# Performance work log

Hardware: AMD Instinct MI355X
Metric: run time of the kernel (lower is better)

Reference implementation:

```python
import jax, jax.numpy as jnp
import numpy as np
import math

B, R, D = 1, 2, 256
NH, NL, NP, ZA = 8, 1, 8, 4
H = W = 128
Q = H * W
HD = D // NH


def _bilinear(v, loc, Hl, Wl):
    # v: [BH, Hl*Wl, hd]; loc: [BH, Q, P, 2] normalized to [0,1]
    x = loc[..., 0] * Wl - 0.5
    y = loc[..., 1] * Hl - 0.5
    x0f = jnp.floor(x); y0f = jnp.floor(y)
    wx = (x - x0f)[..., None]; wy = (y - y0f)[..., None]
    x0 = x0f.astype(jnp.int32); y0 = y0f.astype(jnp.int32)
    def corner(iy, ix):
        valid = (iy >= 0) & (iy < Hl) & (ix >= 0) & (ix < Wl)
        idx = jnp.clip(iy, 0, Hl - 1) * Wl + jnp.clip(ix, 0, Wl - 1)
        g = jax.vmap(lambda vb, ib: vb[ib])(v, idx)  # [BH,Q,P,hd]
        return g * valid[..., None].astype(v.dtype)
    g00 = corner(y0, x0); g01 = corner(y0, x0 + 1)
    g10 = corner(y0 + 1, x0); g11 = corner(y0 + 1, x0 + 1)
    return (g00 * (1 - wx) + g01 * wx) * (1 - wy) + (g10 * (1 - wx) + g11 * wx) * wy


def setup_inputs() -> dict:
    key = jax.random.key(0)
    ks = jax.random.split(key, 12)
    query = jax.random.normal(ks[0], (B, Q, D), jnp.float32)
    value = jax.random.normal(ks[1], (B * R, Q, D), jnp.float32)
    reference_points = jax.random.uniform(ks[2], (R, Q, ZA, 2), jnp.float32)
    spatial_shapes = jnp.array([[H, W]], jnp.int32)
    # sampling_offsets: zero-ish weight + directional grid bias (as in init_weights)
    W_off = 0.01 * jax.random.normal(ks[3], (NH * NL * NP * 2, D), jnp.float32)
    thetas = jnp.arange(NH, dtype=jnp.float32) * (2.0 * math.pi / NH)
    grid = jnp.stack([jnp.cos(thetas), jnp.sin(thetas)], -1)
    grid = grid / jnp.max(jnp.abs(grid), axis=-1, keepdims=True)
    grid = jnp.tile(grid[:, None, None, :], (1, NL, NP, 1))
    grid = grid * (jnp.arange(1, NP + 1, dtype=jnp.float32)[None, None, :, None])
    b_off = grid.reshape(-1)
    W_attn = 0.01 * jax.random.normal(ks[4], (NH * NL * NP, D), jnp.float32)
    b_attn = 0.01 * jax.random.normal(ks[5], (NH * NL * NP,), jnp.float32)
    s = 1.0 / np.sqrt(D)
    W_val = s * jax.random.normal(ks[6], (D, D), jnp.float32)
    b_val = jnp.zeros((D,), jnp.float32)
    W_out = s * jax.random.normal(ks[7], (D, D), jnp.float32)
    b_out = jnp.zeros((D,), jnp.float32)
    return {"query": query, "value": value, "reference_points": reference_points,
            "spatial_shapes": spatial_shapes, "W_off": W_off, "b_off": b_off,
            "W_attn": W_attn, "b_attn": b_attn, "W_val": W_val, "b_val": b_val,
            "W_out": W_out, "b_out": b_out}


def reference(query, value, reference_points, spatial_shapes,
              W_off, b_off, W_attn, b_attn, W_val, b_val, W_out, b_out):
    shapes = np.asarray(spatial_shapes)  # static level shapes
    residual = query
    Bq, nq, d = query.shape
    Rr, _, za, _ = reference_points.shape
    # rebatch query/reference_points over histories -> batch Bq*Rr (== value batch)
    q = jnp.broadcast_to(query[:, None], (Bq, Rr, nq, d)).reshape(Bq * Rr, nq, d)
    rp = jnp.broadcast_to(reference_points[None], (Bq, Rr, nq, za, 2)).reshape(Bq * Rr, nq, za, 2)
    bs = value.shape[0]
    v = (value @ W_val.T + b_val).reshape(bs, -1, NH, HD)
    off = (q @ W_off.T + b_off).reshape(bs, nq, NH, NL, NP, 2)
    aw = jax.nn.softmax((q @ W_attn.T + b_attn).reshape(bs, nq, NH, NL * NP), axis=-1)
    aw = aw.reshape(bs, nq, NH, NL, NP)
    norm = jnp.stack([shapes[:, 1].astype(np.float32), shapes[:, 0].astype(np.float32)], -1)  # [NL,2] = (W,H)
    off = off / norm[None, None, None, :, None, :]
    off = off.reshape(bs, nq, NH, NL, NP // za, za, 2)
    loc = rp[:, :, None, None, None, :, :] + off  # [bs,nq,NH,NL,NP//za,za,2]
    loc = loc.reshape(bs, nq, NH, NL, NP, 2)
    # multi-scale deformable attention (gather + bilinear + weighted sum)
    starts = np.concatenate([[0], np.cumsum(shapes[:, 0] * shapes[:, 1])])
    out = jnp.zeros((bs * NH, nq, HD), v.dtype)
    for l in range(NL):
        Hl, Wl = int(shapes[l, 0]), int(shapes[l, 1])
        vl = v[:, starts[l]:starts[l + 1]].transpose(0, 2, 1, 3).reshape(bs * NH, Hl * Wl, HD)
        locl = loc[:, :, :, l].transpose(0, 2, 1, 3, 4).reshape(bs * NH, nq, NP, 2)
        sampled = _bilinear(vl, locl, Hl, Wl)  # [bs*NH, nq, NP, hd]
        awl = aw[:, :, :, l].transpose(0, 2, 1, 3).reshape(bs * NH, nq, NP)
        out = out + jnp.einsum('bqph,bqp->bqh', sampled, awl)
    out = out.reshape(bs, NH, nq, HD).transpose(0, 2, 1, 3).reshape(bs, nq, d)
    out = out.mean(0, keepdims=True)  # mean over history-batch dim -> [1,nq,d]
    out = out @ W_out.T + b_out
    return out + residual  # dropout is identity in eval
```

## Files before the change

kernel.cpp:

```cpp
#include <hip/hip_runtime.h>
#include <hip/hip_bf16.h>
#include <hip/hip_fp16.h>

#define QN 16384
#define DK 256

typedef float f4_t __attribute__((ext_vector_type(4)));
typedef short s16x8 __attribute__((ext_vector_type(8)));
typedef short s16x4 __attribute__((ext_vector_type(4)));
typedef unsigned int u32;
typedef u32 u32x4 __attribute__((ext_vector_type(4)));
typedef __fp16 h2_t __attribute__((ext_vector_type(2)));

__device__ inline short f2bf(float f){
  __hip_bfloat16 h = __float2bfloat16(f);
  return __builtin_bit_cast(short, h);
}
__device__ inline short f2h16(float f){
  __half h = __float2half(f);
  return __builtin_bit_cast(short, h);
}
__device__ inline float dot2h(u32 a, u32 b, float c){
#if __has_builtin(__builtin_amdgcn_fdot2)
  return __builtin_amdgcn_fdot2(__builtin_bit_cast(h2_t, a),
                                __builtin_bit_cast(h2_t, b), c, false);
#else
  h2_t ha = __builtin_bit_cast(h2_t, a), hb = __builtin_bit_cast(h2_t, b);
  return c + (float)ha[0] * (float)hb[0] + (float)ha[1] * (float)hb[1];
#endif
}
__device__ inline u32 pk2h(float a, float b){
#if __has_builtin(__builtin_amdgcn_cvt_pkrtz)
  h2_t r = __builtin_amdgcn_cvt_pkrtz(a, b);
  return __builtin_bit_cast(u32, r);
#else
  return (u32)__builtin_bit_cast(unsigned short, __float2half(a)) |
         ((u32)__builtin_bit_cast(unsigned short, __float2half(b)) << 16);
#endif
}
__device__ inline u32 bperm(u32 s0, u32 s1, u32 sel){
  return __builtin_amdgcn_perm(s0, s1, sel);
}

__global__ __launch_bounds__(256) void k_convw(const float* __restrict__ Wv,
    const float* __restrict__ Woff, const float* __restrict__ Wattn,
    const float* __restrict__ Wout, short* __restrict__ Wbf){
  const int row = blockIdx.x;
  const int c = threadIdx.x;
  const float* src;
  if (row < 256)       src = Wv    + (size_t)row * DK;
  else if (row < 384)  src = Woff  + (size_t)(row - 256) * DK;
  else if (row < 448)  src = Wattn + (size_t)(row - 384) * DK;
  else                 src = Wout  + (size_t)(row - 448) * DK;
  Wbf[(size_t)row * DK + c] = f2bf(src[c]);
}

__global__ __launch_bounds__(256, 2) void k_gemm_val(const float* __restrict__ A,
    const short* __restrict__ Bw, const float* __restrict__ bval,
    short* __restrict__ vhf){
  __shared__ short As[64 * 256];
  __shared__ short Bs[64 * 256];
  const int tid = threadIdx.x;
  const int lane = tid & 63, wv = tid >> 6;
  const int r16 = lane & 15, kh = lane >> 4;
  const int swsel = (r16 & 7) << 4;
  const int mbase = blockIdx.x * 64;

  #pragma unroll
  for (int i = 0; i < 16; ++i){
    const int lin = i * 256 + tid;
    const int r = lin >> 6, ck = lin & 63;
    const f4_t v = *(const f4_t*)(A + (size_t)(mbase + r) * DK + ck * 4);
    s16x4 o = { f2bf(v[0]), f2bf(v[1]), f2bf(v[2]), f2bf(v[3]) };
    *(s16x4*)((char*)As + r * 512 + ((ck * 8) ^ ((r & 7) << 4))) = o;
  }
  s16x8 breg[8];
  #pragma unroll
  for (int i = 0; i < 8; ++i){
    const int lin = i * 256 + tid;
    const int n = lin >> 5, ck = lin & 31;
    breg[i] = *(const s16x8*)(Bw + (size_t)n * DK + ck * 8);
  }
  __syncthreads();

  for (int cg = 0; cg < 4; ++cg){
    #pragma unroll
    for (int i = 0; i < 8; ++i){
      const int lin = i * 256 + tid;
      const int n = lin >> 5, ck = lin & 31;
      *(s16x8*)((char*)Bs + n * 512 + ((ck * 16) ^ ((n & 7) << 4))) = breg[i];
    }
    __syncthreads();
    if (cg < 3){
      #pragma unroll
      for (int i = 0; i < 8; ++i){
        const int lin = i * 256 + tid;
        const int n = lin >> 5, ck = lin & 31;
        breg[i] = *(const s16x8*)(Bw + (size_t)((cg + 1) * 64 + n) * DK + ck * 8);
      }
    }
    f4_t acc[4];
    #pragma unroll
    for (int i = 0; i < 4; ++i) acc[i] = (f4_t){0.f, 0.f, 0.f, 0.f};
    #pragma unroll
    for (int kk = 0; kk < 8; ++kk){
      const int kb = kh * 16 + kk * 64;
      const s16x8 a = *(const s16x8*)((char*)As + (wv * 16 + r16) * 512 + (kb ^ swsel));
      #pragma unroll
      for (int nt = 0; nt < 4; ++nt){
        const s16x8 b = *(const s16x8*)((char*)Bs + (nt * 16 + r16) * 512 + (kb ^ swsel));
        acc[nt] = __builtin_amdgcn_mfma_f32_16x16x32_bf16(a, b, acc[nt], 0, 0, 0);
      }
    }
    #pragma unroll
    for (int nt = 0; nt < 4; ++nt){
      const int n = cg * 64 + nt * 16 + r16;
      const int h = n >> 5, hd = n & 31;
      const float bv = bval[n];
      #pragma unroll
      for (int rix = 0; rix < 4; ++rix){
        const int m = mbase + wv * 16 + kh * 4 + rix;
        const int r = m >> 14, pix = m & (QN - 1);
        vhf[(size_t)((r * 8 + h) * QN + pix) * 32 + hd] = f2h16(acc[nt][rix] + bv);
      }
    }
    __syncthreads();
  }
}

__global__ __launch_bounds__(256, 2) void k_gemm_oa(const float* __restrict__ A,
    const short* __restrict__ Bw, const float* __restrict__ boff,
    const float* __restrict__ battn, float* __restrict__ offw,
    float* __restrict__ logit){
  __shared__ short As[32 * 256];
  __shared__ short Bs[64 * 256];
  const int tid = threadIdx.x;
  const int lane = tid & 63, wv = tid >> 6;
  const int r16 = lane & 15, kh = lane >> 4;
  const int mg = wv & 1, ch = wv >> 1;
  const int swsel = (r16 & 7) << 4;
  const int mbase = blockIdx.x * 32;

  #pragma unroll
  for (int i = 0; i < 8; ++i){
    const int lin = i * 256 + tid;
    const int r = lin >> 6, ck = lin & 63;
    const f4_t v = *(const f4_t*)(A + (size_t)(mbase + r) * DK + ck * 4);
    s16x4 o = { f2bf(v[0]), f2bf(v[1]), f2bf(v[2]), f2bf(v[3]) };
    *(s16x4*)((char*)As + r * 512 + ((ck * 8) ^ ((r & 7) << 4))) = o;
  }
  s16x8 breg[8];
  #pragma unroll
  for (int i = 0; i < 8; ++i){
    const int lin = i * 256 + tid;
    const int n = lin >> 5, ck = lin & 31;
    breg[i] = *(const s16x8*)(Bw + (size_t)n * DK + ck * 8);
  }
  __syncthreads();

  for (int cg = 0; cg < 3; ++cg){
    #pragma unroll
    for (int i = 0; i < 8; ++i){
      const int lin = i * 256 + tid;
      const int n = lin >> 5, ck = lin & 31;
      *(s16x8*)((char*)Bs + n * 512 + ((ck * 16) ^ ((n & 7) << 4))) = breg[i];
    }
    __syncthreads();
    if (cg < 2){
      #pragma unroll
      for (int i = 0; i < 8; ++i){
        const int lin = i * 256 + tid;
        const int n = lin >> 5, ck = lin & 31;
        breg[i] = *(const s16x8*)(Bw + (size_t)((cg + 1) * 64 + n) * DK + ck * 8);
      }
    }
    f4_t acc[2];
    acc[0] = (f4_t){0.f,0.f,0.f,0.f}; acc[1] = (f4_t){0.f,0.f,0.f,0.f};
    #pragma unroll
    for (int kk = 0; kk < 8; ++kk){
      const int kb = kh * 16 + kk * 64;
      const s16x8 a = *(const s16x8*)((char*)As + (mg * 16 + r16) * 512 + (kb ^ swsel));
      #pragma unroll
      for (int nt = 0; nt < 2; ++nt){
        const s16x8 b = *(const s16x8*)((char*)Bs + (ch * 32 + nt * 16 + r16) * 512 + (kb ^ swsel));
        acc[nt] = __builtin_amdgcn_mfma_f32_16x16x32_bf16(a, b, acc[nt], 0, 0, 0);
      }
    }
    #pragma unroll
    for (int nt = 0; nt < 2; ++nt){
      const int n = cg * 64 + ch * 32 + nt * 16 + r16;
      #pragma unroll
      for (int rix = 0; rix < 4; ++rix){
        const int m = mbase + mg * 16 + kh * 4 + rix;
        const float v = acc[nt][rix];
        if (n < 128) offw[(size_t)m * 128 + n] = v + boff[n];
        else         logit[(size_t)m * 64 + (n - 128)] = v + battn[n - 128];
      }
    }
    __syncthreads();
  }
}

__global__ __launch_bounds__(256, 2) void k_gemm_out(const float* __restrict__ A,
    const short* __restrict__ Bw, const float* __restrict__ bout,
    const float* __restrict__ query, float* __restrict__ out){
  __shared__ short As[32 * 256];
  __shared__ short Bs[64 * 256];
  const int tid = threadIdx.x;
  const int lane = tid & 63, wv = tid >> 6;
  const int r16 = lane & 15, kh = lane >> 4;
  const int mg = wv & 1, ch = wv >> 1;
  const int swsel = (r16 & 7) << 4;
  const int mbase = blockIdx.x * 32;

  #pragma unroll
  for (int i = 0; i < 8; ++i){
    const int lin = i * 256 + tid;
    const int r = lin >> 6, ck = lin & 63;
    const f4_t v = *(const f4_t*)(A + (size_t)(mbase + r) * DK + ck * 4);
    s16x4 o = { f2bf(v[0]), f2bf(v[1]), f2bf(v[2]), f2bf(v[3]) };
    *(s16x4*)((char*)As + r * 512 + ((ck * 8) ^ ((r & 7) << 4))) = o;
  }
  s16x8 breg[8];
  #pragma unroll
  for (int i = 0; i < 8; ++i){
    const int lin = i * 256 + tid;
    const int n = lin >> 5, ck = lin & 31;
    breg[i] = *(const s16x8*)(Bw + (size_t)n * DK + ck * 8);
  }
  __syncthreads();

  for (int cg = 0; cg < 4; ++cg){
    #pragma unroll
    for (int i = 0; i < 8; ++i){
      const int lin = i * 256 + tid;
      const int n = lin >> 5, ck = lin & 31;
      *(s16x8*)((char*)Bs + n * 512 + ((ck * 16) ^ ((n & 7) << 4))) = breg[i];
    }
    __syncthreads();
    if (cg < 3){
      #pragma unroll
      for (int i = 0; i < 8; ++i){
        const int lin = i * 256 + tid;
        const int n = lin >> 5, ck = lin & 31;
        breg[i] = *(const s16x8*)(Bw + (size_t)((cg + 1) * 64 + n) * DK + ck * 8);
      }
    }
    f4_t acc[2];
    acc[0] = (f4_t){0.f,0.f,0.f,0.f}; acc[1] = (f4_t){0.f,0.f,0.f,0.f};
    #pragma unroll
    for (int kk = 0; kk < 8; ++kk){
      const int kb = kh * 16 + kk * 64;
      const s16x8 a = *(const s16x8*)((char*)As + (mg * 16 + r16) * 512 + (kb ^ swsel));
      #pragma unroll
      for (int nt = 0; nt < 2; ++nt){
        const s16x8 b = *(const s16x8*)((char*)Bs + (ch * 32 + nt * 16 + r16) * 512 + (kb ^ swsel));
        acc[nt] = __builtin_amdgcn_mfma_f32_16x16x32_bf16(a, b, acc[nt], 0, 0, 0);
      }
    }
    #pragma unroll
    for (int nt = 0; nt < 2; ++nt){
      const int n = cg * 64 + ch * 32 + nt * 16 + r16;
      const float bo = bout[n];
      #pragma unroll
      for (int rix = 0; rix < 4; ++rix){
        const int m = mbase + mg * 16 + kh * 4 + rix;
        out[(size_t)m * DK + n] = acc[nt][rix] + bo + query[(size_t)m * DK + n];
      }
    }
    __syncthreads();
  }
}

__device__ inline void mkw(float rx, float ry, float ox, float oy, float awp,
                           u32& word, u32& pk01, u32& pk23){
  const float x = fmaf(rx, 128.f, ox) - 0.5f;
  const float y = fmaf(ry, 128.f, oy) - 0.5f;
  const float xf = floorf(x), yf = floorf(y);
  const float wx = x - xf, wy = y - yf;
  const int ix = (int)xf, iy = (int)yf;
  float xw0 = 1.f - wx, xw1 = wx, yw0 = 1.f - wy, yw1 = wy;
  if (ix < 0 || ix > 127)   xw0 = 0.f;
  if (ix < -1 || ix > 126)  xw1 = 0.f;
  if (iy < 0 || iy > 127)   yw0 = 0.f;
  if (iy < -1 || iy > 126)  yw1 = 0.f;
  const int ix0 = min(max(ix, 0), 127), ix1 = min(max(ix + 1, 0), 127);
  const int iy0 = min(max(iy, 0), 127), iy1 = min(max(iy + 1, 0), 127);
  const float t0 = awp * yw0, t1 = awp * yw1;
  pk01 = pk2h(t0 * xw0, t0 * xw1);
  pk23 = pk2h(t1 * xw0, t1 * xw1);
  word = (u32)(iy0 * 128 + ix0) | ((u32)(ix1 - ix0) << 16) | ((u32)(iy1 - iy0) << 17);
}

__global__ __launch_bounds__(256) void k_sampler(const float* __restrict__ rp,
    const float* __restrict__ offw, const float* __restrict__ logit,
    const short* __restrict__ vhf, float* __restrict__ O2){
  const int tid = threadIdx.x;
  const int j = tid & 3;
  const int grp = tid >> 2;
  const int lane = tid & 63;
  const int glane = lane & ~3;
  const int h = blockIdx.x & 7;
  const int q = (blockIdx.x >> 3) * 64 + grp;
  const u32 jof = (u32)j * 8;

  const float* lp = logit + (size_t)q * 64 + h * 8;
  const float l0 = lp[0], l1 = lp[1], l2 = lp[2], l3 = lp[3];
  const float l4 = lp[4], l5 = lp[5], l6 = lp[6], l7 = lp[7];
  float mx = fmaxf(fmaxf(fmaxf(l0, l1), fmaxf(l2, l3)),
                   fmaxf(fmaxf(l4, l5), fmaxf(l6, l7)));
  float sum = __expf(l0 - mx) + __expf(l1 - mx) + __expf(l2 - mx) + __expf(l3 - mx)
            + __expf(l4 - mx) + __expf(l5 - mx) + __expf(l6 - mx) + __expf(l7 - mx);
  const float sc = 0.5f / sum;
  const float wA = __expf(lp[j] - mx) * sc;
  const float wB = __expf(lp[j + 4] - mx) * sc;

  const float* offp = offw + (size_t)q * 128 + h * 16;
  const float ox0 = offp[2 * j],     oy0 = offp[2 * j + 1];
  const float ox1 = offp[2 * j + 8], oy1 = offp[2 * j + 9];
  const float* rp0 = rp + (size_t)q * 8 + j * 2;
  const float* rp1 = rp + (size_t)(QN + q) * 8 + j * 2;
  const float rx0 = rp0[0], ry0 = rp0[1];
  const float rx1 = rp1[0], ry1 = rp1[1];

  u32 wrd0, pk01_0, pk23_0, wrd1, pk01_1, pk23_1;
  u32 wrd2, pk01_2, pk23_2, wrd3, pk01_3, pk23_3;
  mkw(rx0, ry0, ox0, oy0, wA, wrd0, pk01_0, pk23_0);
  mkw(rx0, ry0, ox1, oy1, wB, wrd1, pk01_1, pk23_1);
  mkw(rx1, ry1, ox0, oy0, wA, wrd2, pk01_2, pk23_2);
  mkw(rx1, ry1, ox1, oy1, wB, wrd3, pk01_3, pk23_3);

  const short* vb0 = vhf + (size_t)(h * QN) * 32;
  const short* vb1 = vhf + (size_t)((8 + h) * QN) * 32;

  float acc[8] = {0.f,0.f,0.f,0.f,0.f,0.f,0.f,0.f};

#define STEP(S, WRD, PK01, PK23) do{                                        \
    const int srcl_ = glane | ((S) & 3);                                    \
    const u32 w01_ = __shfl((PK01), srcl_);                                 \
    const u32 w23_ = __shfl((PK23), srcl_);                                 \
    const u32 wd_  = __shfl((WRD),  srcl_);                                 \
    const u32 o00_ = (wd_ & 0xFFFFu) * 32u + jof;                           \
    const u32 o01_ = o00_ + ((wd_ >> 11) & 32u);                            \
    const u32 dy_  = (wd_ >> 17) & 1u;                                      \
    const u32 o10_ = o00_ + dy_ * 4096u;                                    \
    const u32 o11_ = o01_ + dy_ * 4096u;                                    \
    const short* vb_ = ((S) >> 3) ? vb1 : vb0;                              \
    const u32x4 c00_ = *(const u32x4*)(vb_ + o00_);                         \
    const u32x4 c01_ = *(const u32x4*)(vb_ + o01_);                         \
    const u32x4 c10_ = *(const u32x4*)(vb_ + o10_);                         \
    const u32x4 c11_ = *(const u32x4*)(vb_ + o11_);                         \
    _Pragma("unroll")                                                       \
    for (int e = 0; e < 4; ++e){                                            \
      const u32 p0_ = bperm(c01_[e], c00_[e], 0x05040100u);                 \
      const u32 p1_ = bperm(c01_[e], c00_[e], 0x07060302u);                 \
      const u32 q0_ = bperm(c11_[e], c10_[e], 0x05040100u);                 \
      const u32 q1_ = bperm(c11_[e], c10_[e], 0x07060302u);                 \
      acc[2*e]   = dot2h(p0_, w01_, acc[2*e]);                              \
      acc[2*e+1] = dot2h(p1_, w01_, acc[2*e+1]);                            \
      acc[2*e]   = dot2h(q0_, w23_, acc[2*e]);                              \
      acc[2*e+1] = dot2h(q1_, w23_, acc[2*e+1]);                            \
    }                                                                       \
  }while(0)

  STEP(0,  wrd0, pk01_0, pk23_0); STEP(1,  wrd0, pk01_0, pk23_0);
  STEP(2,  wrd0, pk01_0, pk23_0); STEP(3,  wrd0, pk01_0, pk23_0);
  STEP(4,  wrd1, pk01_1, pk23_1); STEP(5,  wrd1, pk01_1, pk23_1);
  STEP(6,  wrd1, pk01_1, pk23_1); STEP(7,  wrd1, pk01_1, pk23_1);
  STEP(8,  wrd2, pk01_2, pk23_2); STEP(9,  wrd2, pk01_2, pk23_2);
  STEP(10, wrd2, pk01_2, pk23_2); STEP(11, wrd2, pk01_2, pk23_2);
  STEP(12, wrd3, pk01_3, pk23_3); STEP(13, wrd3, pk01_3, pk23_3);
  STEP(14, wrd3, pk01_3, pk23_3); STEP(15, wrd3, pk01_3, pk23_3);
#undef STEP

  float* op = O2 + (size_t)q * DK + h * 32 + j * 8;
  *(f4_t*)op       = (f4_t){acc[0], acc[1], acc[2], acc[3]};
  *(f4_t*)(op + 4) = (f4_t){acc[4], acc[5], acc[6], acc[7]};
}

extern "C" void kernel_launch(void* const* d_in, const int* in_sizes, int n_in,
                              void* d_out, int out_size, void* d_ws, size_t ws_size,
                              hipStream_t stream) {
  const float* query = (const float*)d_in[0];
  const float* value = (const float*)d_in[1];
  const float* refpt = (const float*)d_in[2];
  const float* W_off  = (const float*)d_in[4];
  const float* b_off  = (const float*)d_in[5];
  const float* W_attn = (const float*)d_in[6];
  const float* b_attn = (const float*)d_in[7];
  const float* W_val  = (const float*)d_in[8];
  const float* b_val  = (const float*)d_in[9];
  const float* W_out  = (const float*)d_in[10];
  const float* b_out  = (const float*)d_in[11];
  float* out = (float*)d_out;

  char* ws = (char*)d_ws;
  short* Wbf  = (short*)(ws);
  short* vhf  = (short*)(ws + 360448);
  float* offw = (float*)(ws + 17137664);
  float* logit= (float*)(ws + 25526272);
  float* O2   = (float*)(ws + 29720576);

  k_convw   <<<dim3(704),  dim3(256), 0, stream>>>(W_val, W_off, W_attn, W_out, Wbf);
  k_gemm_val<<<dim3(512),  dim3(256), 0, stream>>>(value, Wbf, b_val, vhf);
  k_gemm_oa <<<dim3(512),  dim3(256), 0, stream>>>(query, Wbf + 256 * DK, b_off, b_attn, offw, logit);
  k_sampler <<<dim3(2048), dim3(256), 0, stream>>>(refpt, offw, logit, vhf, O2);
  k_gemm_out<<<dim3(512),  dim3(256), 0, stream>>>(O2, Wbf + 448 * DK, b_out, query, out);
}
```

Measured before the change: 79.37 us.

## Split sampler corner gathers across lane pairs and store bf16 intermediate

The sampler now assigns 8 threads per query-head instead of 4. Each lane pair splits the x-corners of a sample, so every lane loads two corners instead of four, and the partial sums are combined with a shuffle. The softmax over the 8 logits becomes a shuffle reduction, and the grid doubles to 4096 blocks. The sampler output is also written as bf16 instead of fp32, which halves that write and lets the output GEMM load bf16 directly without converting. In exchange the kernel does more shuffles and half the lanes sit idle at the store.

```diff
diff --git a/kernel.cpp b/kernel.cpp
--- a/kernel.cpp
+++ b/kernel.cpp
@@ -201,7 +201,7 @@
   }
 }
 
-__global__ __launch_bounds__(256, 2) void k_gemm_out(const float* __restrict__ A,
+__global__ __launch_bounds__(256, 2) void k_gemm_out(const short* __restrict__ Ab,
     const short* __restrict__ Bw, const float* __restrict__ bout,
     const float* __restrict__ query, float* __restrict__ out){
   __shared__ short As[32 * 256];
@@ -214,12 +214,11 @@
   const int mbase = blockIdx.x * 32;
 
   #pragma unroll
-  for (int i = 0; i < 8; ++i){
-    const int lin = i * 256 + tid;
-    const int r = lin >> 6, ck = lin & 63;
-    const f4_t v = *(const f4_t*)(A + (size_t)(mbase + r) * DK + ck * 4);
-    s16x4 o = { f2bf(v[0]), f2bf(v[1]), f2bf(v[2]), f2bf(v[3]) };
-    *(s16x4*)((char*)As + r * 512 + ((ck * 8) ^ ((r & 7) << 4))) = o;
+  for (int i = 0; i < 4; ++i){
+    const int lin = i * 256 + tid;
+    const int r = lin >> 5, ck = lin & 31;
+    const s16x8 v = *(const s16x8*)(Ab + (size_t)(mbase + r) * DK + ck * 8);
+    *(s16x8*)((char*)As + r * 512 + ((ck * 16) ^ ((r & 7) << 4))) = v;
   }
   s16x8 breg[8];
   #pragma unroll
@@ -294,88 +293,80 @@
 
 __global__ __launch_bounds__(256) void k_sampler(const float* __restrict__ rp,
     const float* __restrict__ offw, const float* __restrict__ logit,
-    const short* __restrict__ vhf, float* __restrict__ O2){
+    const short* __restrict__ vhf, short* __restrict__ O2b){
   const int tid = threadIdx.x;
-  const int j = tid & 3;
-  const int grp = tid >> 2;
+  const int j3 = tid & 7;
+  const int cj = j3 & 3;
+  const int px = j3 >> 2;
+  const int grp = tid >> 3;
   const int lane = tid & 63;
-  const int glane = lane & ~3;
+  const int glane8 = lane & ~7;
   const int h = blockIdx.x & 7;
-  const int q = (blockIdx.x >> 3) * 64 + grp;
-  const u32 jof = (u32)j * 8;
+  const int q = (blockIdx.x >> 3) * 32 + grp;
+  const u32 cjof = (u32)cj * 8;
+  const u32 selw = px ? 0x03020706u : 0x01000504u;
 
   const float* lp = logit + (size_t)q * 64 + h * 8;
-  const float l0 = lp[0], l1 = lp[1], l2 = lp[2], l3 = lp[3];
-  const float l4 = lp[4], l5 = lp[5], l6 = lp[6], l7 = lp[7];
-  float mx = fmaxf(fmaxf(fmaxf(l0, l1), fmaxf(l2, l3)),
-                   fmaxf(fmaxf(l4, l5), fmaxf(l6, l7)));
-  float sum = __expf(l0 - mx) + __expf(l1 - mx) + __expf(l2 - mx) + __expf(l3 - mx)
-            + __expf(l4 - mx) + __expf(l5 - mx) + __expf(l6 - mx) + __expf(l7 - mx);
-  const float sc = 0.5f / sum;
-  const float wA = __expf(lp[j] - mx) * sc;
-  const float wB = __expf(lp[j + 4] - mx) * sc;
+  const float l = lp[j3];
+  float m = l;
+  m = fmaxf(m, __shfl_xor(m, 1)); m = fmaxf(m, __shfl_xor(m, 2)); m = fmaxf(m, __shfl_xor(m, 4));
+  const float e = __expf(l - m);
+  float ssum = e;
+  ssum += __shfl_xor(ssum, 1); ssum += __shfl_xor(ssum, 2); ssum += __shfl_xor(ssum, 4);
+  const float awp = e * (0.5f / ssum);
 
   const float* offp = offw + (size_t)q * 128 + h * 16;
-  const float ox0 = offp[2 * j],     oy0 = offp[2 * j + 1];
-  const float ox1 = offp[2 * j + 8], oy1 = offp[2 * j + 9];
-  const float* rp0 = rp + (size_t)q * 8 + j * 2;
-  const float* rp1 = rp + (size_t)(QN + q) * 8 + j * 2;
-  const float rx0 = rp0[0], ry0 = rp0[1];
-  const float rx1 = rp1[0], ry1 = rp1[1];
-
-  u32 wrd0, pk01_0, pk23_0, wrd1, pk01_1, pk23_1;
-  u32 wrd2, pk01_2, pk23_2, wrd3, pk01_3, pk23_3;
-  mkw(rx0, ry0, ox0, oy0, wA, wrd0, pk01_0, pk23_0);
-  mkw(rx0, ry0, ox1, oy1, wB, wrd1, pk01_1, pk23_1);
-  mkw(rx1, ry1, ox0, oy0, wA, wrd2, pk01_2, pk23_2);
-  mkw(rx1, ry1, ox1, oy1, wB, wrd3, pk01_3, pk23_3);
+  const float ox = offp[2 * j3], oy = offp[2 * j3 + 1];
+  const int za2 = (j3 & 3) * 2;
+  const float rx0 = rp[(size_t)q * 8 + za2],        ry0 = rp[(size_t)q * 8 + za2 + 1];
+  const float rx1 = rp[(size_t)(QN + q) * 8 + za2], ry1 = rp[(size_t)(QN + q) * 8 + za2 + 1];
+
+  u32 wrdA, pkA01, pkA23, wrdB, pkB01, pkB23;
+  mkw(rx0, ry0, ox, oy, awp, wrdA, pkA01, pkA23);
+  mkw(rx1, ry1, ox, oy, awp, wrdB, pkB01, pkB23);
 
   const short* vb0 = vhf + (size_t)(h * QN) * 32;
   const short* vb1 = vhf + (size_t)((8 + h) * QN) * 32;
 
   float acc[8] = {0.f,0.f,0.f,0.f,0.f,0.f,0.f,0.f};
 
-#define STEP(S, WRD, PK01, PK23) do{                                        \
-    const int srcl_ = glane | ((S) & 3);                                    \
+#define STEP(S, WRD, PK01, PK23, VB) do{                                    \
+    const int srcl_ = glane8 | ((S) & 7);                                   \
+    const u32 wd_  = __shfl((WRD),  srcl_);                                 \
     const u32 w01_ = __shfl((PK01), srcl_);                                 \
     const u32 w23_ = __shfl((PK23), srcl_);                                 \
-    const u32 wd_  = __shfl((WRD),  srcl_);                                 \
-    const u32 o00_ = (wd_ & 0xFFFFu) * 32u + jof;                           \
-    const u32 o01_ = o00_ + ((wd_ >> 11) & 32u);                            \
-    const u32 dy_  = (wd_ >> 17) & 1u;                                      \
-    const u32 o10_ = o00_ + dy_ * 4096u;                                    \
-    const u32 o11_ = o01_ + dy_ * 4096u;                                    \
-    const short* vb_ = ((S) >> 3) ? vb1 : vb0;                              \
-    const u32x4 c00_ = *(const u32x4*)(vb_ + o00_);                         \
-    const u32x4 c01_ = *(const u32x4*)(vb_ + o01_);                         \
-    const u32x4 c10_ = *(const u32x4*)(vb_ + o10_);                         \
-    const u32x4 c11_ = *(const u32x4*)(vb_ + o11_);                         \
+    const u32 wp_  = bperm(w01_, w23_, selw);     \
+    const u32 o0_  = (wd_ & 0xFFFFu) * 32u + cjof                           \
+                   + (px ? ((wd_ >> 11) & 32u) : 0u);                       \
+    const u32 o1_  = o0_ + ((wd_ >> 17) & 1u) * 4096u;                      \
+    const u32x4 cA_ = *(const u32x4*)((VB) + o0_);              \
+    const u32x4 cB_ = *(const u32x4*)((VB) + o1_);              \
     _Pragma("unroll")                                                       \
-    for (int e = 0; e < 4; ++e){                                            \
-      const u32 p0_ = bperm(c01_[e], c00_[e], 0x05040100u);                 \
-      const u32 p1_ = bperm(c01_[e], c00_[e], 0x07060302u);                 \
-      const u32 q0_ = bperm(c11_[e], c10_[e], 0x05040100u);                 \
-      const u32 q1_ = bperm(c11_[e], c10_[e], 0x07060302u);                 \
-      acc[2*e]   = dot2h(p0_, w01_, acc[2*e]);                              \
-      acc[2*e+1] = dot2h(p1_, w01_, acc[2*e+1]);                            \
-      acc[2*e]   = dot2h(q0_, w23_, acc[2*e]);                              \
-      acc[2*e+1] = dot2h(q1_, w23_, acc[2*e+1]);                            \
+    for (int e_ = 0; e_ < 4; ++e_){                                         \
+      const u32 pl_ = bperm(cA_[e_], cB_[e_], 0x01000504u);                 \
+      const u32 ph_ = bperm(cA_[e_], cB_[e_], 0x03020706u);                 \
+      acc[2*e_]   = dot2h(pl_, wp_, acc[2*e_]);                             \
+      acc[2*e_+1] = dot2h(ph_, wp_, acc[2*e_+1]);                           \
     }                                                                       \
   }while(0)
 
-  STEP(0,  wrd0, pk01_0, pk23_0); STEP(1,  wrd0, pk01_0, pk23_0);
-  STEP(2,  wrd0, pk01_0, pk23_0); STEP(3,  wrd0, pk01_0, pk23_0);
-  STEP(4,  wrd1, pk01_1, pk23_1); STEP(5,  wrd1, pk01_1, pk23_1);
-  STEP(6,  wrd1, pk01_1, pk23_1); STEP(7,  wrd1, pk01_1, pk23_1);
-  STEP(8,  wrd2, pk01_2, pk23_2); STEP(9,  wrd2, pk01_2, pk23_2);
-  STEP(10, wrd2, pk01_2, pk23_2); STEP(11, wrd2, pk01_2, pk23_2);
-  STEP(12, wrd3, pk01_3, pk23_3); STEP(13, wrd3, pk01_3, pk23_3);
-  STEP(14, wrd3, pk01_3, pk23_3); STEP(15, wrd3, pk01_3, pk23_3);
+  STEP(0,  wrdA, pkA01, pkA23, vb0); STEP(1,  wrdA, pkA01, pkA23, vb0);
+  STEP(2,  wrdA, pkA01, pkA23, vb0); STEP(3,  wrdA, pkA01, pkA23, vb0);
+  STEP(4,  wrdA, pkA01, pkA23, vb0); STEP(5,  wrdA, pkA01, pkA23, vb0);
+  STEP(6,  wrdA, pkA01, pkA23, vb0); STEP(7,  wrdA, pkA01, pkA23, vb0);
+  STEP(8,  wrdB, pkB01, pkB23, vb1); STEP(9,  wrdB, pkB01, pkB23, vb1);
+  STEP(10, wrdB, pkB01, pkB23, vb1); STEP(11, wrdB, pkB01, pkB23, vb1);
+  STEP(12, wrdB, pkB01, pkB23, vb1); STEP(13, wrdB, pkB01, pkB23, vb1);
+  STEP(14, wrdB, pkB01, pkB23, vb1); STEP(15, wrdB, pkB01, pkB23, vb1);
 #undef STEP
 
-  float* op = O2 + (size_t)q * DK + h * 32 + j * 8;
-  *(f4_t*)op       = (f4_t){acc[0], acc[1], acc[2], acc[3]};
-  *(f4_t*)(op + 4) = (f4_t){acc[4], acc[5], acc[6], acc[7]};
+  #pragma unroll
+  for (int i = 0; i < 8; ++i) acc[i] += __shfl_xor(acc[i], 4);
+  if (px == 0){
+    s16x8 o = { f2bf(acc[0]), f2bf(acc[1]), f2bf(acc[2]), f2bf(acc[3]),
+                f2bf(acc[4]), f2bf(acc[5]), f2bf(acc[6]), f2bf(acc[7]) };
+    *(s16x8*)(O2b + (size_t)q * DK + h * 32 + cj * 8) = o;
+  }
 }
 
 extern "C" void kernel_launch(void* const* d_in, const int* in_sizes, int n_in,
@@ -399,11 +390,11 @@
   short* vhf  = (short*)(ws + 360448);
   float* offw = (float*)(ws + 17137664);
   float* logit= (float*)(ws + 25526272);
-  float* O2   = (float*)(ws + 29720576);
+  short* O2b  = (short*)(ws + 29720576);
 
   k_convw   <<<dim3(704),  dim3(256), 0, stream>>>(W_val, W_off, W_attn, W_out, Wbf);
   k_gemm_val<<<dim3(512),  dim3(256), 0, stream>>>(value, Wbf, b_val, vhf);
   k_gemm_oa <<<dim3(512),  dim3(256), 0, stream>>>(query, Wbf + 256 * DK, b_off, b_attn, offw, logit);
-  k_sampler <<<dim3(2048), dim3(256), 0, stream>>>(refpt, offw, logit, vhf, O2);
-  k_gemm_out<<<dim3(512),  dim3(256), 0, stream>>>(O2, Wbf + 448 * DK, b_out, query, out);
-}
+  k_sampler <<<dim3(4096), dim3(256), 0, stream>>>(refpt, offw, logit, vhf, O2b);
+  k_gemm_out<<<dim3(512),  dim3(256), 0, stream>>>(O2b, Wbf + 448 * DK, b_out, query, out);
+}
```

Result: faster. 75.63 us (-4.7%).
